# Kernel tuning notes

Hardware: AMD Instinct MI355X
Metric: run time of the kernel (lower is better)

The kernel has to match this reference:

```python
import jax, jax.numpy as jnp
import numpy as np

E = 200000          # number of edges (nodes of the line graph)
NNZ = 1600000       # nonzeros of the edge-to-edge sparse adjacency
EF = 16             # edge_feat_dim
M = 128             # message_dim


def setup_inputs() -> dict:
    key = jax.random.key(0)
    ks = jax.random.split(key, 12)
    inp = {
        "edge_feat": jax.random.normal(ks[0], (E, EF), jnp.float32),
        "message_old": jax.random.normal(ks[1], (E, M), jnp.float32),
        "adj_rows": jax.random.randint(ks[2], (NNZ,), 0, E, jnp.int32),
        "adj_cols": jax.random.randint(ks[3], (NNZ,), 0, E, jnp.int32),
        "adj_vals": jax.random.uniform(ks[4], (NNZ,), jnp.float32),
        # message_edge_lin: Linear(EF+M -> M)
        "W1": jax.random.normal(ks[5], (M, EF + M), jnp.float32) / np.sqrt(EF + M),
        "b1": jnp.zeros((M,), jnp.float32),
        # message_pass_lin: Linear(M -> M)
        "W2": jax.random.normal(ks[6], (M, M), jnp.float32) / np.sqrt(M),
        "b2": jnp.zeros((M,), jnp.float32),
        # GRUCell(M, M)
        "W_ih": jax.random.normal(ks[7], (3 * M, M), jnp.float32) / np.sqrt(M),
        "W_hh": jax.random.normal(ks[8], (3 * M, M), jnp.float32) / np.sqrt(M),
        "b_ih": jax.random.normal(ks[9], (3 * M,), jnp.float32) * 0.01,
        "b_hh": jax.random.normal(ks[10], (3 * M,), jnp.float32) * 0.01,
    }
    return inp


def reference(edge_feat, message_old, adj_rows, adj_cols, adj_vals,
              W1, b1, W2, b2, W_ih, W_hh, b_ih, b_hh):
    # message_edge_lin(cat(message_old, edge_feat)) + ReLU
    x = jnp.concatenate([message_old, edge_feat], axis=1)      # [E, M+EF]
    msg = jax.nn.relu(x @ W1.T + b1)                           # [E, M]
    # torch.sparse.mm(nb_adj, msg): out[r] += val * msg[c]
    gathered = msg[adj_cols] * adj_vals[:, None]               # [NNZ, M]
    msg = jax.ops.segment_sum(gathered, adj_rows, num_segments=E)
    # message_pass_lin + ReLU
    msg = jax.nn.relu(msg @ W2.T + b2)                         # [E, M]
    # GRUCell(input=msg, hidden=message_old), torch semantics
    gi = msg @ W_ih.T + b_ih                                   # [E, 3M]
    gh = message_old @ W_hh.T + b_hh                           # [E, 3M]
    i_r, i_z, i_n = jnp.split(gi, 3, axis=1)
    h_r, h_z, h_n = jnp.split(gh, 3, axis=1)
    r = jax.nn.sigmoid(i_r + h_r)
    z = jax.nn.sigmoid(i_z + h_z)
    n = jnp.tanh(i_n + r * h_n)
    return (1.0 - z) * n + z * message_old
```

## Files before the change

kernel.cpp:

```cpp
#include <hip/hip_runtime.h>
#include <hip/hip_bf16.h>


typedef __attribute__((ext_vector_type(4))) float f32x4;
typedef __attribute__((ext_vector_type(8))) short s16x8;

#define MDIM 128
#define EFDIM 16
#define K1PAD 160
#define SCAN_BLK 1024

__device__ __forceinline__ ushort f2bf(float f) {
  union { float f; unsigned u; } v; v.f = f;
  unsigned u = v.u;
  unsigned r = (u + 0x7fffu + ((u >> 16) & 1u)) >> 16;
  return (ushort)r;
}
__device__ __forceinline__ float bf2f(ushort h) {
  union { unsigned u; float f; } v; v.u = ((unsigned)h) << 16; return v.f;
}
__device__ __forceinline__ short f2bfn(float f) {
  __hip_bfloat16 h = __float2bfloat16(f);
  return *reinterpret_cast<short*>(&h);
}
__device__ __forceinline__ s16x8 cvt8n(f32x4 a, f32x4 b) {
  s16x8 o;
  o[0] = f2bfn(a[0]); o[1] = f2bfn(a[1]); o[2] = f2bfn(a[2]); o[3] = f2bfn(a[3]);
  o[4] = f2bfn(b[0]); o[5] = f2bfn(b[1]); o[6] = f2bfn(b[2]); o[7] = f2bfn(b[3]);
  return o;
}
__device__ __forceinline__ s16x8 cvt8m(f32x4 a, f32x4 b) {
  s16x8 o;
  o[0] = (short)f2bf(a[0]); o[1] = (short)f2bf(a[1]);
  o[2] = (short)f2bf(a[2]); o[3] = (short)f2bf(a[3]);
  o[4] = (short)f2bf(b[0]); o[5] = (short)f2bf(b[1]);
  o[6] = (short)f2bf(b[2]); o[7] = (short)f2bf(b[3]);
  return o;
}
__device__ __forceinline__ f32x4 mfma16(s16x8 a, s16x8 b, f32x4 c) {
  return __builtin_amdgcn_mfma_f32_16x16x32_bf16(a, b, c, 0, 0, 0);
}
__device__ __forceinline__ float sigmoidf_(float x) { return 1.f / (1.f + __expf(-x)); }
__device__ __forceinline__ float tanhf_(float x) {
  float xc = fminf(fmaxf(x, -15.f), 15.f);
  float t = __expf(2.f * xc);
  return (t - 1.f) / (t + 1.f);
}

__global__ __launch_bounds__(256) void prep_kernel(
    const float* __restrict__ W1, const float* __restrict__ W2,
    const float* __restrict__ Wih, const float* __restrict__ Whh,
    ushort* __restrict__ W1b, ushort* __restrict__ W2b,
    ushort* __restrict__ Wihb, ushort* __restrict__ Whhb) {
  int idx = blockIdx.x * 256 + threadIdx.x;
  if (idx < 128 * K1PAD) {
    int n = idx / K1PAD, k = idx % K1PAD;
    W1b[idx] = (k < 144) ? f2bf(W1[n * 144 + k]) : (ushort)0;
    return;
  }
  int i2 = idx - 128 * K1PAD;
  if (i2 < 128 * 128) { W2b[i2] = f2bf(W2[i2]); return; }
  int i3 = i2 - 128 * 128;
  if (i3 < 384 * 128) { Wihb[i3] = f2bf(Wih[i3]); return; }
  int i4 = i3 - 384 * 128;
  if (i4 < 384 * 128) { Whhb[i4] = f2bf(Whh[i4]); return; }
}

__global__ __launch_bounds__(256) void linear1_kernel(
    const float* __restrict__ mo, const float* __restrict__ ef,
    const ushort* __restrict__ W1b, const float* __restrict__ b1,
    ushort* __restrict__ msg1b) {
  __shared__ ushort w1l[5 * 4096];
  const int tid = threadIdx.x;
  const int wave = tid >> 6, lane = tid & 63;
  const int r = lane & 15, kg = lane >> 4;
  const int row0 = blockIdx.x * 64 + wave * 16;
  const int arow = row0 + r;

#pragma unroll
  for (int l = 0; l < 10; ++l) {
    const int gid = l * 256 + tid;
    const int stp = gid >> 9, col = (gid >> 2) & 127, kgs = gid & 3;
    uint4 v = *(const uint4*)(W1b + col * K1PAD + stp * 32 + kgs * 8);
    *(uint4*)&w1l[gid * 8] = v;
  }
  __syncthreads();

  f32x4 acc[8] = {};
#pragma unroll
  for (int step = 0; step < 5; ++step) {
    const int k0 = step * 32 + kg * 8;
    s16x8 a;
    if (k0 < 128) {
      f32x4 f1 = *(const f32x4*)(mo + (size_t)arow * MDIM + k0);
      f32x4 f2 = *(const f32x4*)(mo + (size_t)arow * MDIM + k0 + 4);
      a = cvt8n(f1, f2);
    } else if (k0 < 144) {
      f32x4 f1 = *(const f32x4*)(ef + (size_t)arow * EFDIM + (k0 - 128));
      f32x4 f2 = *(const f32x4*)(ef + (size_t)arow * EFDIM + (k0 - 128) + 4);
      a = cvt8n(f1, f2);
    } else {
      a = (s16x8){0, 0, 0, 0, 0, 0, 0, 0};
    }
#pragma unroll
    for (int f = 0; f < 8; ++f) {
      s16x8 b = *(const s16x8*)&w1l[step * 4096 + (f * 16 + r) * 32 + kg * 8];
      acc[f] = mfma16(a, b, acc[f]);
    }
  }
#pragma unroll
  for (int f = 0; f < 8; ++f) {
    const int col = f * 16 + r;
    const float bias = b1[col];
#pragma unroll
    for (int j = 0; j < 4; ++j) {
      const int orow = row0 + kg * 4 + j;
      float v = acc[f][j] + bias;
      v = v > 0.f ? v : 0.f;
      msg1b[(size_t)orow * MDIM + col] = f2bf(v);
    }
  }
}

__global__ __launch_bounds__(256) void hist_kernel(const int* __restrict__ rows,
                                                   int* __restrict__ cnt, int nnz) {
  int i = blockIdx.x * 256 + threadIdx.x;
  if (i < nnz) atomicAdd(&cnt[rows[i]], 1);
}

__global__ __launch_bounds__(256) void scan1_kernel(const int* __restrict__ cnt,
                                                    int* __restrict__ excl,
                                                    int* __restrict__ bsums, int n) {
  __shared__ int wsum[4];
  const int t = threadIdx.x;
  const int base = blockIdx.x * SCAN_BLK + t * 4;
  int v[4];
#pragma unroll
  for (int j = 0; j < 4; ++j) v[j] = (base + j < n) ? cnt[base + j] : 0;
  const int s = v[0] + v[1] + v[2] + v[3];
  const int lane = t & 63, wave = t >> 6;
  int inc = s;
#pragma unroll
  for (int d = 1; d < 64; d <<= 1) {
    int o = __shfl_up(inc, d, 64);
    if (lane >= d) inc += o;
  }
  if (lane == 63) wsum[wave] = inc;
  __syncthreads();
  int woff = 0;
#pragma unroll
  for (int wv = 0; wv < 4; ++wv) if (wv < wave) woff += wsum[wv];
  int run = woff + inc - s;
#pragma unroll
  for (int j = 0; j < 4; ++j) {
    if (base + j < n) excl[base + j] = run;
    run += v[j];
  }
  if (t == 0) bsums[blockIdx.x] = wsum[0] + wsum[1] + wsum[2] + wsum[3];
}

__global__ __launch_bounds__(256) void scan2_kernel(int* __restrict__ bsums, int nb) {
  __shared__ int ws[4];
  const int t = threadIdx.x;
  const int v = (t < nb) ? bsums[t] : 0;
  const int lane = t & 63, wave = t >> 6;
  int inc = v;
#pragma unroll
  for (int d = 1; d < 64; d <<= 1) {
    int o = __shfl_up(inc, d, 64);
    if (lane >= d) inc += o;
  }
  if (lane == 63) ws[wave] = inc;
  __syncthreads();
  int woff = 0;
#pragma unroll
  for (int wv = 0; wv < 4; ++wv) if (wv < wave) woff += ws[wv];
  if (t < nb) bsums[t] = woff + inc - v;
}

__global__ __launch_bounds__(256) void scatter_kernel(
    const int* __restrict__ rows, const int* __restrict__ cols,
    const float* __restrict__ vals, const int* __restrict__ excl,
    const int* __restrict__ bsums, int* __restrict__ row_fill,
    int2* __restrict__ csr, int nnz) {
  int i = blockIdx.x * 256 + threadIdx.x;
  if (i >= nnz) return;
  int r = rows[i];
  int base = excl[r] + bsums[r >> 10];
  int idx = base + atomicAdd(&row_fill[r], 1);
  int2 cv;
  cv.x = cols[i];
  cv.y = __float_as_int(vals[i]);
  csr[idx] = cv;
}

__global__ __launch_bounds__(256) void gather_kernel(
    const int* __restrict__ excl, const int* __restrict__ bsums,
    const int2* __restrict__ csr,
    const ushort* __restrict__ msg1b, ushort* __restrict__ msg2b,
    int E, int nnz) {
  const int w = (blockIdx.x * 256 + threadIdx.x) >> 6;
  if (w >= E) return;
  const int lane = threadIdx.x & 63;
  const int sub = lane >> 4, c = lane & 15;
  const int start = excl[w] + bsums[w >> 10];
  const int end = (w + 1 < E) ? (excl[w + 1] + bsums[(w + 1) >> 10]) : nnz;

  float acc[8] = {};
  int j = start + sub;
  if (j < end) {
    int2 cv = csr[j];
    while (true) {
      const int jn = j + 4;
      const bool more = jn < end;
      int2 cvn = cv;
      if (more) cvn = csr[jn];
      const float val = __int_as_float(cv.y);
      const s16x8 m = *(const s16x8*)(msg1b + (size_t)cv.x * MDIM + c * 8);
#pragma unroll
      for (int t = 0; t < 8; ++t) acc[t] += bf2f((ushort)m[t]) * val;
      if (!more) break;
      cv = cvn;
      j = jn;
    }
  }
#pragma unroll
  for (int t = 0; t < 8; ++t) {
    acc[t] += __shfl_xor(acc[t], 16, 64);
    acc[t] += __shfl_xor(acc[t], 32, 64);
  }
  if (sub == 0) {
    s16x8 o;
#pragma unroll
    for (int t = 0; t < 8; ++t) o[t] = (short)f2bf(acc[t]);
    *(s16x8*)(msg2b + (size_t)w * MDIM + c * 8) = o;
  }
}

__global__ __launch_bounds__(256) void msg3_kernel(
    const ushort* __restrict__ msg2b, const ushort* __restrict__ W2b,
    const float* __restrict__ b2, ushort* __restrict__ msg3b) {
  __shared__ ushort w2l[4 * 4096];
  const int tid = threadIdx.x;
  const int wave = tid >> 6, lane = tid & 63;
  const int r = lane & 15, kg = lane >> 4;
  const int row0 = blockIdx.x * 64 + wave * 16;

#pragma unroll
  for (int l = 0; l < 8; ++l) {
    const int gid = l * 256 + tid;
    const int stp = gid >> 9, col = (gid >> 2) & 127, kgs = gid & 3;
    uint4 v = *(const uint4*)(W2b + col * MDIM + stp * 32 + kgs * 8);
    *(uint4*)&w2l[gid * 8] = v;
  }

  s16x8 a1[4];
#pragma unroll
  for (int step = 0; step < 4; ++step)
    a1[step] = *(const s16x8*)(msg2b + (size_t)(row0 + r) * MDIM + step * 32 + kg * 8);
  __syncthreads();

  f32x4 acc[8] = {};
#pragma unroll
  for (int step = 0; step < 4; ++step) {
#pragma unroll
    for (int f = 0; f < 8; ++f) {
      s16x8 b = *(const s16x8*)&w2l[step * 4096 + (f * 16 + r) * 32 + kg * 8];
      acc[f] = mfma16(a1[step], b, acc[f]);
    }
  }
#pragma unroll
  for (int f = 0; f < 8; ++f) {
    const int col = f * 16 + r;
    const float bias = b2[col];
#pragma unroll
    for (int j = 0; j < 4; ++j) {
      const int orow = row0 + kg * 4 + j;
      float v = acc[f][j] + bias;
      v = v > 0.f ? v : 0.f;
      msg3b[(size_t)orow * MDIM + col] = f2bf(v);
    }
  }
}

__global__ __launch_bounds__(512, 4) void gate_kernel(
    const ushort* __restrict__ msg3b, const float* __restrict__ mo,
    const ushort* __restrict__ Wihb, const ushort* __restrict__ Whhb,
    const float* __restrict__ bih, const float* __restrict__ bhh,
    float* __restrict__ out, int E) {
  __shared__ ushort wl[6 * 4096];
  const int tid = threadIdx.x;

  const int nwg = gridDim.x;
  const int orig = blockIdx.x;
  const int q = nwg >> 3, rm = nwg & 7;
  const int xcd = orig & 7, bidx = orig >> 3;
  const int wgid = (xcd < rm ? xcd * (q + 1) : rm * (q + 1) + (xcd - rm) * q) + bidx;
  const int cg = wgid & 3;
  const int row0 = (wgid >> 2) * 128;

  const int wave = tid >> 6, lane = tid & 63;
  const int r = lane & 15, kg = lane >> 4;

  const int lr = tid >> 4, g = tid & 15;
#pragma unroll
  for (int l = 0; l < 6; ++l) {
    const ushort* src = (l & 1) ? Whhb : Wihb;
    const int gate = l >> 1;
    uint4 v = *(const uint4*)(src + (size_t)(gate * 128 + cg * 32 + lr) * MDIM + g * 8);
    *(uint4*)&wl[l * 4096 + lr * 128 + ((g * 8) ^ ((lr & 7) << 3))] = v;
  }

  const int arow0 = row0 + wave * 16 + r;
  const int arow = arow0 < E ? arow0 : E - 1;
  s16x8 ai[4], ah[4];
#pragma unroll
  for (int step = 0; step < 4; ++step) {
    const int k0 = step * 32 + kg * 8;
    ai[step] = *(const s16x8*)(msg3b + (size_t)arow * MDIM + k0);
    f32x4 f1 = *(const f32x4*)(mo + (size_t)arow * MDIM + k0);
    f32x4 f2 = *(const f32x4*)(mo + (size_t)arow * MDIM + k0 + 4);
    ah[step] = cvt8m(f1, f2);
  }
  __syncthreads();

  float outv[8];
#pragma unroll
  for (int p = 0; p < 2; ++p) {
    const int slr = p * 16 + r;
    f32x4 a_ir = {}, a_hr = {}, a_iz = {}, a_hz = {}, a_in = {}, a_hn = {};
#pragma unroll
    for (int step = 0; step < 4; ++step) {
      const int k0 = step * 32 + kg * 8;
      const int sw = slr * 128 + (k0 ^ ((slr & 7) << 3));
      s16x8 b_ir = *(const s16x8*)&wl[0 * 4096 + sw];
      s16x8 b_hr = *(const s16x8*)&wl[1 * 4096 + sw];
      a_ir = mfma16(ai[step], b_ir, a_ir);
      a_hr = mfma16(ah[step], b_hr, a_hr);
      s16x8 b_iz = *(const s16x8*)&wl[2 * 4096 + sw];
      s16x8 b_hz = *(const s16x8*)&wl[3 * 4096 + sw];
      a_iz = mfma16(ai[step], b_iz, a_iz);
      a_hz = mfma16(ah[step], b_hz, a_hz);
      s16x8 b_in = *(const s16x8*)&wl[4 * 4096 + sw];
      s16x8 b_hn = *(const s16x8*)&wl[5 * 4096 + sw];
      a_in = mfma16(ai[step], b_in, a_in);
      a_hn = mfma16(ah[step], b_hn, a_hn);
    }
    const int c128 = cg * 32 + p * 16 + r;
    const float bi_r = bih[c128], bh_r = bhh[c128];
    const float bi_z = bih[128 + c128], bh_z = bhh[128 + c128];
    const float bi_n = bih[256 + c128], bh_n = bhh[256 + c128];
#pragma unroll
    for (int j = 0; j < 4; ++j) {
      const int orow0 = row0 + wave * 16 + kg * 4 + j;
      const int orow = orow0 < E ? orow0 : E - 1;
      const float rr_ = sigmoidf_((a_ir[j] + bi_r) + (a_hr[j] + bh_r));
      const float zz = sigmoidf_((a_iz[j] + bi_z) + (a_hz[j] + bh_z));
      const float nn = tanhf_((a_in[j] + bi_n) + rr_ * (a_hn[j] + bh_n));
      const float m = mo[(size_t)orow * MDIM + c128];
      outv[p * 4 + j] = (1.f - zz) * nn + zz * m;
    }
  }

#pragma unroll
  for (int p = 0; p < 2; ++p) {
    const int c128 = cg * 32 + p * 16 + r;
#pragma unroll
    for (int j = 0; j < 4; ++j) {
      const int orow = row0 + wave * 16 + kg * 4 + j;
      if (orow < E)
        __builtin_nontemporal_store(outv[p * 4 + j], out + (size_t)orow * MDIM + c128);
    }
  }
}

extern "C" void kernel_launch(void* const* d_in, const int* in_sizes, int n_in,
                              void* d_out, int out_size, void* d_ws, size_t ws_size,
                              hipStream_t stream) {
  const float* ef   = (const float*)d_in[0];
  const float* mo   = (const float*)d_in[1];
  const int*   arow = (const int*)d_in[2];
  const int*   acol = (const int*)d_in[3];
  const float* aval = (const float*)d_in[4];
  const float* W1   = (const float*)d_in[5];
  const float* b1   = (const float*)d_in[6];
  const float* W2   = (const float*)d_in[7];
  const float* b2   = (const float*)d_in[8];
  const float* Wih  = (const float*)d_in[9];
  const float* Whh  = (const float*)d_in[10];
  const float* bih  = (const float*)d_in[11];
  const float* bhh  = (const float*)d_in[12];
  float* out = (float*)d_out;

  const int E   = in_sizes[0] / EFDIM;
  const int nnz = in_sizes[2];

  char* w = (char*)d_ws;
  size_t off = 0;
  ushort* msg1b   = (ushort*)(w + off); off += (size_t)E * MDIM * 2;
  ushort* msg2b   = (ushort*)(w + off); off += (size_t)E * MDIM * 2;
  ushort* msg3b   = (ushort*)(w + off); off += (size_t)E * MDIM * 2;
  int*    row_cnt = (int*)(w + off);    off += (size_t)E * 4;
  int*    row_fill= (int*)(w + off);    off += (size_t)E * 4;
  int*    excl    = (int*)(w + off);    off += (size_t)E * 4;
  int*    bsums   = (int*)(w + off);    off += 256 * 4;
  int2*   csr     = (int2*)(w + off);   off += (size_t)nnz * 8;
  ushort* W1b     = (ushort*)(w + off); off += 128 * K1PAD * 2;
  ushort* W2b     = (ushort*)(w + off); off += 128 * 128 * 2;
  ushort* Wihb    = (ushort*)(w + off); off += 384 * 128 * 2;
  ushort* Whhb    = (ushort*)(w + off); off += 384 * 128 * 2;
  if (off > ws_size) return;

  const int prep_elems = 128 * K1PAD + 128 * 128 + 2 * 384 * 128;
  prep_kernel<<<(prep_elems + 255) / 256, 256, 0, stream>>>(W1, W2, Wih, Whh,
                                                            W1b, W2b, Wihb, Whhb);
  linear1_kernel<<<E / 64, 256, 0, stream>>>(mo, ef, W1b, b1, msg1b);

  hipMemsetAsync(row_cnt, 0, (size_t)E * 8, stream);
  hist_kernel<<<(nnz + 255) / 256, 256, 0, stream>>>(arow, row_cnt, nnz);
  const int nscan = (E + SCAN_BLK - 1) / SCAN_BLK;
  scan1_kernel<<<nscan, 256, 0, stream>>>(row_cnt, excl, bsums, E);
  scan2_kernel<<<1, 256, 0, stream>>>(bsums, nscan);
  scatter_kernel<<<(nnz + 255) / 256, 256, 0, stream>>>(arow, acol, aval, excl, bsums,
                                                        row_fill, csr, nnz);

  {
    const long long total = (long long)E * 64;
    const int grid = (int)((total + 255) / 256);
    gather_kernel<<<grid, 256, 0, stream>>>(excl, bsums, csr, msg1b, msg2b, E, nnz);
  }

  msg3_kernel<<<E / 64, 256, 0, stream>>>(msg2b, W2b, b2, msg3b);
  {
    const int nrt = (E + 127) / 128;
    gate_kernel<<<nrt * 4, 512, 0, stream>>>(msg3b, mo, Wihb, Whhb, bih, bhh, out, E);
  }
}
```

Before: 405.8 us.

## Fuse sparse gather with message_pass linear via shared-memory tile

Merges the CSR gather (sparse mm) and the W2 linear+ReLU into one kernel. Each 64-row block first gathers its rows into a padded LDS tile, then runs the MFMA matmul directly from LDS. This removes the msg2 round trip through global memory and one launch. In exchange, each wave now loops serially over 16 rows and the block uses more LDS, which may reduce occupancy and latency hiding for the irregular gather.

```diff
diff --git a/kernel.cpp b/kernel.cpp
--- a/kernel.cpp
+++ b/kernel.cpp
@@ -194,57 +194,16 @@
   csr[idx] = cv;
 }
 
-__global__ __launch_bounds__(256) void gather_kernel(
+__global__ __launch_bounds__(256) void gather_msg3_kernel(
     const int* __restrict__ excl, const int* __restrict__ bsums,
-    const int2* __restrict__ csr,
-    const ushort* __restrict__ msg1b, ushort* __restrict__ msg2b,
-    int E, int nnz) {
-  const int w = (blockIdx.x * 256 + threadIdx.x) >> 6;
-  if (w >= E) return;
-  const int lane = threadIdx.x & 63;
-  const int sub = lane >> 4, c = lane & 15;
-  const int start = excl[w] + bsums[w >> 10];
-  const int end = (w + 1 < E) ? (excl[w + 1] + bsums[(w + 1) >> 10]) : nnz;
-
-  float acc[8] = {};
-  int j = start + sub;
-  if (j < end) {
-    int2 cv = csr[j];
-    while (true) {
-      const int jn = j + 4;
-      const bool more = jn < end;
-      int2 cvn = cv;
-      if (more) cvn = csr[jn];
-      const float val = __int_as_float(cv.y);
-      const s16x8 m = *(const s16x8*)(msg1b + (size_t)cv.x * MDIM + c * 8);
-#pragma unroll
-      for (int t = 0; t < 8; ++t) acc[t] += bf2f((ushort)m[t]) * val;
-      if (!more) break;
-      cv = cvn;
-      j = jn;
-    }
-  }
-#pragma unroll
-  for (int t = 0; t < 8; ++t) {
-    acc[t] += __shfl_xor(acc[t], 16, 64);
-    acc[t] += __shfl_xor(acc[t], 32, 64);
-  }
-  if (sub == 0) {
-    s16x8 o;
-#pragma unroll
-    for (int t = 0; t < 8; ++t) o[t] = (short)f2bf(acc[t]);
-    *(s16x8*)(msg2b + (size_t)w * MDIM + c * 8) = o;
-  }
-}
-
-__global__ __launch_bounds__(256) void msg3_kernel(
-    const ushort* __restrict__ msg2b, const ushort* __restrict__ W2b,
-    const float* __restrict__ b2, ushort* __restrict__ msg3b) {
+    const int2* __restrict__ csr, const ushort* __restrict__ msg1b,
+    const ushort* __restrict__ W2b, const float* __restrict__ b2,
+    ushort* __restrict__ msg3b, int E, int nnz) {
   __shared__ ushort w2l[4 * 4096];
+  __shared__ ushort m2[64][136];
   const int tid = threadIdx.x;
   const int wave = tid >> 6, lane = tid & 63;
-  const int r = lane & 15, kg = lane >> 4;
-  const int row0 = blockIdx.x * 64 + wave * 16;
+  const int row0 = blockIdx.x * 64;
 
 #pragma unroll
   for (int l = 0; l < 8; ++l) {
@@ -254,11 +213,50 @@
     *(uint4*)&w2l[gid * 8] = v;
   }
 
+  const int sub = lane >> 4, c = lane & 15;
+  for (int i = 0; i < 16; ++i) {
+    const int local = wave * 16 + i;
+    const int w = row0 + local;
+    const int start = excl[w] + bsums[w >> 10];
+    const int end = (w + 1 < E) ? (excl[w + 1] + bsums[(w + 1) >> 10]) : nnz;
+
+    float acc[8] = {};
+    int j = start + sub;
+    if (j < end) {
+      int2 cv = csr[j];
+      while (true) {
+        const int jn = j + 4;
+        const bool more = jn < end;
+        int2 cvn = cv;
+        if (more) cvn = csr[jn];
+        const float val = __int_as_float(cv.y);
+        const s16x8 m = *(const s16x8*)(msg1b + (size_t)cv.x * MDIM + c * 8);
+#pragma unroll
+        for (int t = 0; t < 8; ++t) acc[t] += bf2f((ushort)m[t]) * val;
+        if (!more) break;
+        cv = cvn;
+        j = jn;
+      }
+    }
+#pragma unroll
+    for (int t = 0; t < 8; ++t) {
+      acc[t] += __shfl_xor(acc[t], 16, 64);
+      acc[t] += __shfl_xor(acc[t], 32, 64);
+    }
+    if (sub == 0) {
+      s16x8 o;
+#pragma unroll
+      for (int t = 0; t < 8; ++t) o[t] = (short)f2bf(acc[t]);
+      *(s16x8*)&m2[local][c * 8] = o;
+    }
+  }
+  __syncthreads();
+
+  const int r = lane & 15, kg = lane >> 4;
   s16x8 a1[4];
 #pragma unroll
   for (int step = 0; step < 4; ++step)
-    a1[step] = *(const s16x8*)(msg2b + (size_t)(row0 + r) * MDIM + step * 32 + kg * 8);
-  __syncthreads();
+    a1[step] = *(const s16x8*)&m2[wave * 16 + r][step * 32 + kg * 8];
 
   f32x4 acc[8] = {};
 #pragma unroll
@@ -275,7 +273,7 @@
     const float bias = b2[col];
 #pragma unroll
     for (int j = 0; j < 4; ++j) {
-      const int orow = row0 + kg * 4 + j;
+      const int orow = row0 + wave * 16 + kg * 4 + j;
       float v = acc[f][j] + bias;
       v = v > 0.f ? v : 0.f;
       msg3b[(size_t)orow * MDIM + col] = f2bf(v);
@@ -398,7 +396,6 @@
   char* w = (char*)d_ws;
   size_t off = 0;
   ushort* msg1b   = (ushort*)(w + off); off += (size_t)E * MDIM * 2;
-  ushort* msg2b   = (ushort*)(w + off); off += (size_t)E * MDIM * 2;
   ushort* msg3b   = (ushort*)(w + off); off += (size_t)E * MDIM * 2;
   int*    row_cnt = (int*)(w + off);    off += (size_t)E * 4;
   int*    row_fill= (int*)(w + off);    off += (size_t)E * 4;
@@ -424,13 +421,9 @@
   scatter_kernel<<<(nnz + 255) / 256, 256, 0, stream>>>(arow, acol, aval, excl, bsums,
                                                         row_fill, csr, nnz);
 
-  {
-    const long long total = (long long)E * 64;
-    const int grid = (int)((total + 255) / 256);
-    gather_kernel<<<grid, 256, 0, stream>>>(excl, bsums, csr, msg1b, msg2b, E, nnz);
-  }
-
-  msg3_kernel<<<E / 64, 256, 0, stream>>>(msg2b, W2b, b2, msg3b);
+  gather_msg3_kernel<<<E / 64, 256, 0, stream>>>(excl, bsums, csr, msg1b, W2b, b2,
+                                                 msg3b, E, nnz);
+
   {
     const int nrt = (E + 127) / 128;
     gate_kernel<<<nrt * 4, 512, 0, stream>>>(msg3b, mo, Wihb, Whhb, bih, bhh, out, E);
```

New measurement: 466.5 us. +15.0%, slower.
